# Kernel optimization log

Hardware: AMD Instinct MI355X
Metric: run time of the kernel (lower is better)

The kernel has to match this reference:

```python
import jax, jax.numpy as jnp
import numpy as np

ALPHA, BETA = 0.7, 0.3   # cost weights from match_to_memory
MARGIN = 1.0             # contrastive margin
EPS = 1e-12

N, M, D = 4096, 10240, 256

def setup_inputs() -> dict:
    key = jax.random.key(0)
    k1, k2, k3, k4, k5, k6 = jax.random.split(key, 6)
    return {
        "curr_embeds": jax.random.normal(k1, (N, D), dtype=jnp.float32),
        "curr_boxes": jax.random.uniform(k2, (N, 4), dtype=jnp.float32),
        "prev_embeds": jax.random.normal(k3, (M, D), dtype=jnp.float32),
        "prev_boxes": jax.random.uniform(k4, (M, 4), dtype=jnp.float32),
        "curr_ids": jax.random.randint(k5, (N,), 0, 5000, dtype=jnp.int64) if jax.config.read('jax_enable_x64') else jax.random.randint(k5, (N,), 0, 5000, dtype=jnp.int32),
        "prev_ids": jax.random.randint(k6, (M,), 0, 5000, dtype=jnp.int32),
    }

def _centers(boxes):
    # boxes: [K,4] as (x, y, w, h) -> centers [K,2]
    x, y, w, h = boxes[:, 0], boxes[:, 1], boxes[:, 2], boxes[:, 3]
    return jnp.stack([x + w / 2, y + h / 2], axis=-1)

def _pairwise_dist(a, b):
    # Euclidean cdist via expansion; avoids [N,M,D] intermediate.
    a2 = jnp.sum(a * a, axis=-1, keepdims=True)        # [N,1]
    b2 = jnp.sum(b * b, axis=-1, keepdims=True).T      # [1,M]
    d2 = jnp.maximum(a2 + b2 - 2.0 * (a @ b.T), 0.0)   # [N,M]
    return jnp.sqrt(d2), d2

def reference(curr_embeds, curr_boxes, prev_embeds, prev_boxes, curr_ids, prev_ids):
    # --- cost matrix (match_to_memory, pre-Hungarian) ---
    cn = curr_embeds / jnp.maximum(jnp.linalg.norm(curr_embeds, axis=1, keepdims=True), EPS)
    pn = prev_embeds / jnp.maximum(jnp.linalg.norm(prev_embeds, axis=1, keepdims=True), EPS)
    cost_sim = 1.0 - cn @ pn.T                                   # [N,M]
    cost_center, _ = _pairwise_dist(_centers(curr_boxes), _centers(prev_boxes))
    total_cost = ALPHA * cost_sim + BETA * cost_center           # [N,M]

    # --- contrastive loss (vectorized form of the O(N*M) python loop) ---
    dist, d2 = _pairwise_dist(curr_embeds, prev_embeds)          # [N,M]
    same = curr_ids[:, None] == prev_ids[None, :]                # [N,M] bool
    per_pair = jnp.where(same, d2, jnp.maximum(MARGIN - dist, 0.0) ** 2)
    loss = jnp.sum(per_pair) / (dist.shape[0] * dist.shape[1])
    return total_cost, loss
```

## Files before the change

### kernel.cpp

```cpp
#include <hip/hip_runtime.h>
#include <hip/hip_bf16.h>

#define N_CURR 4096
#define M_PREV 10240
#define DIM 256
#define BM 128
#define BN 128
#define BK2 64
#define NBX (M_PREV / BN)
#define NBY (N_CURR / BM)
#define NBLK (NBX * NBY)

typedef short short8 __attribute__((ext_vector_type(8)));
typedef float f32x4 __attribute__((ext_vector_type(4)));

__device__ __forceinline__ unsigned short f2bf(float f) {
  union { float f; unsigned int u; } x; x.f = f;
  unsigned int u = x.u;
  return (unsigned short)((u + 0x7fffu + ((u >> 16) & 1u)) >> 16);
}

__device__ __forceinline__ void async16(const void* g, void* l) {
  __builtin_amdgcn_global_load_lds(
      (const __attribute__((address_space(1))) unsigned int*)g,
      (__attribute__((address_space(3))) unsigned int*)l, 16, 0, 0);
}

__global__ __launch_bounds__(256) void prep_kernel(
    const float* __restrict__ ce, const float* __restrict__ cbx,
    const float* __restrict__ pe, const float* __restrict__ pbx,
    ushort* __restrict__ cbf, ushort* __restrict__ pbf,
    float4* __restrict__ cpar, float4* __restrict__ ppar)
{
  int gw = (blockIdx.x * 256 + threadIdx.x) >> 6;
  int lane = threadIdx.x & 63;
  bool isCurr = gw < N_CURR;
  int row = isCurr ? gw : gw - N_CURR;
  const float* src = (isCurr ? ce : pe) + (size_t)row * DIM;
  ushort* dst = (isCurr ? cbf : pbf) + (size_t)row * DIM;

  float4 v = ((const float4*)src)[lane];
  ushort4 b;
  b.x = f2bf(v.x); b.y = f2bf(v.y); b.z = f2bf(v.z); b.w = f2bf(v.w);
  ((ushort4*)dst)[lane] = b;

  float s = v.x*v.x + v.y*v.y + v.z*v.z + v.w*v.w;
  #pragma unroll
  for (int m = 32; m; m >>= 1) s += __shfl_xor(s, m);

  if (lane == 0) {
    float nrm = fmaxf(__builtin_amdgcn_sqrtf(s), 1e-12f);
    float4 bb = ((const float4*)(isCurr ? cbx : pbx))[row];
    float4 par;
    par.x = 1.0f / nrm;
    par.y = s;
    par.z = bb.x + 0.5f * bb.z;
    par.w = bb.y + 0.5f * bb.w;
    (isCurr ? cpar : ppar)[row] = par;
  }
}

__global__ __launch_bounds__(512, 4) void main_kernel(
    const ushort* __restrict__ cbf, const ushort* __restrict__ pbf,
    const float4* __restrict__ cpar, const float4* __restrict__ ppar,
    const int* __restrict__ cid, const int* __restrict__ pid,
    float* __restrict__ out, float* __restrict__ partials)
{
  __shared__ __align__(16) ushort Al[2][BM][BK2];
  __shared__ __align__(16) ushort Bl[2][BN][BK2];
  __shared__ float4 rowv[BM];
  __shared__ float4 colv[BN];
  __shared__ int ridl[BM];
  __shared__ int cidl[BN];
  __shared__ float wsum[8];

  const int bid = blockIdx.x;
  const int bx = bid % NBX;
  const int by = bid / NBX;
  const int r0 = by * BM;
  const int c0 = bx * BN;
  const int tid = threadIdx.x;
  const int lane = tid & 63;
  const int wid = tid >> 6;

  const int sr = lane >> 3;
  const int sc = ((lane & 7) ^ sr) * 8;

  auto stage = [&](int buf, int ks) {
    const int k0 = ks * BK2;
    const int rA = wid * 16 + sr;
    const ushort* gA = cbf + (size_t)(r0 + rA) * DIM + k0 + sc;
    async16(gA,           &Al[buf][wid*16][0]);
    async16(gA + 8*DIM,   &Al[buf][wid*16 + 8][0]);
    const ushort* gB = pbf + (size_t)(c0 + rA) * DIM + k0 + sc;
    async16(gB,           &Bl[buf][wid*16][0]);
    async16(gB + 8*DIM,   &Bl[buf][wid*16 + 8][0]);
  };

  stage(0, 0);

  if (tid < BM) {
    rowv[tid] = cpar[r0 + tid];
    ridl[tid] = cid[r0 + tid];
  } else if (tid < 2 * BM) {
    int t = tid - BM;
    float4 pv = ppar[c0 + t];
    pv.x *= 0.7f;
    colv[t] = pv;
    cidl[t] = pid[c0 + t];
  }

  f32x4 acc[2][4];
  #pragma unroll
  for (int n = 0; n < 2; ++n)
    #pragma unroll
    for (int m = 0; m < 4; ++m)
      acc[n][m] = (f32x4){0.f, 0.f, 0.f, 0.f};

  const int wr = wid >> 2, wc = wid & 3;
  const int rb = wr * 64, cbase = wc * 32;
  const int frow = lane & 15;
  const int f7 = frow & 7;
  const int cko = lane >> 4;

  #pragma unroll
  for (int ks = 0; ks < DIM / BK2; ++ks) {
    __syncthreads();
    if (ks < DIM / BK2 - 1) stage((ks + 1) & 1, ks + 1);
    const int buf = ks & 1;
    #pragma unroll
    for (int half = 0; half < 2; ++half) {
      const int cc = ((half * 4 + cko) ^ f7) * 16;
      short8 af[4], bfr[2];
      #pragma unroll
      for (int m = 0; m < 4; ++m)
        af[m] = *(const short8*)((const char*)&Al[buf][rb + m*16 + frow][0] + cc);
      #pragma unroll
      for (int n = 0; n < 2; ++n)
        bfr[n] = *(const short8*)((const char*)&Bl[buf][cbase + n*16 + frow][0] + cc);
      #pragma unroll
      for (int n = 0; n < 2; ++n)
        #pragma unroll
        for (int m = 0; m < 4; ++m)
          acc[n][m] = __builtin_amdgcn_mfma_f32_16x16x32_bf16(bfr[n], af[m], acc[n][m], 0, 0, 0);
    }
  }

  float lp = 0.f;
  const int g4 = (lane >> 4) << 2;
  #pragma unroll
  for (int m = 0; m < 4; ++m) {
    int il = rb + m*16 + frow;
    float4 rv = rowv[il];
    int rid = ridl[il];
    float* orow = out + (size_t)(r0 + il) * M_PREV + c0;
    #pragma unroll
    for (int n = 0; n < 2; ++n) {
      int jl0 = cbase + n*16 + g4;
      f32x4 res;
      #pragma unroll
      for (int r = 0; r < 4; ++r) {
        int jl = jl0 + r;
        float4 cv = colv[jl];
        float dot = acc[n][m][r];
        float w = rv.x * cv.x;
        float dx = rv.z - cv.z;
        float dy = rv.w - cv.w;
        float ccd = __builtin_amdgcn_sqrtf(dx*dx + dy*dy);
        res[r] = fmaf(0.3f, ccd, fmaf(-w, dot, 0.7f));
        float d2 = fmaxf(rv.y + cv.y - 2.0f * dot, 0.0f);
        float dist = __builtin_amdgcn_sqrtf(d2);
        float tt = fmaxf(1.0f - dist, 0.0f);
        lp += (rid == cidl[jl]) ? d2 : tt * tt;
      }
      *(f32x4*)(orow + jl0) = res;
    }
  }

  #pragma unroll
  for (int m = 32; m; m >>= 1) lp += __shfl_xor(lp, m);
  if (lane == 0) wsum[wid] = lp;
  __syncthreads();
  if (tid == 0) {
    float s = 0.f;
    #pragma unroll
    for (int w = 0; w < 8; ++w) s += wsum[w];
    partials[bid] = s;
  }
}

__global__ __launch_bounds__(256) void finalize_loss(
    const float* __restrict__ partials, float* __restrict__ loss_out)
{
  __shared__ float sh[4];
  float s = 0.f;
  for (int i = threadIdx.x; i < NBLK; i += 256) s += partials[i];
  #pragma unroll
  for (int m = 32; m; m >>= 1) s += __shfl_xor(s, m);
  if ((threadIdx.x & 63) == 0) sh[threadIdx.x >> 6] = s;
  __syncthreads();
  if (threadIdx.x == 0)
    loss_out[0] = ((sh[0] + sh[1]) + (sh[2] + sh[3])) * (1.0f / 41943040.0f);
}

extern "C" void kernel_launch(void* const* d_in, const int* in_sizes, int n_in,
                              void* d_out, int out_size, void* d_ws, size_t ws_size,
                              hipStream_t stream) {
  const float* ce  = (const float*)d_in[0];
  const float* cbx = (const float*)d_in[1];
  const float* pe  = (const float*)d_in[2];
  const float* pbx = (const float*)d_in[3];
  const int*   cid = (const int*)d_in[4];
  const int*   pid = (const int*)d_in[5];
  float* out = (float*)d_out;

  char* ws = (char*)d_ws;
  ushort* cbf = (ushort*)ws;
  ushort* pbf = (ushort*)(ws + (2u << 20));
  float4* cpar = (float4*)(ws + 7340032);
  float4* ppar = (float4*)(ws + 7340032 + 65536);
  float* partials = (float*)(ws + 7340032 + 65536 + 163840);

  prep_kernel<<<(N_CURR + M_PREV) / 4, 256, 0, stream>>>(
      ce, cbx, pe, pbx, cbf, pbf, cpar, ppar);
  main_kernel<<<NBLK, 512, 0, stream>>>(
      cbf, pbf, cpar, ppar, cid, pid, out, partials);
  finalize_loss<<<1, 256, 0, stream>>>(partials, out + (size_t)N_CURR * M_PREV);
}
```

Baseline: 68.55 us.

## Load B fragments directly into registers and swizzle block order across XCDs

The B operand tile no longer goes through LDS. Each wave loads its own B fragments straight from global memory into registers, double-buffered one k-step ahead. The A tile is still staged asynchronously into LDS, now synchronised with a manual vmcnt wait and a raw barrier. Block IDs are remapped so that contiguous tiles land on the same XCD, which should improve L2 reuse. The changes aim to cut LDS traffic and barrier cost, but they duplicate B global loads across the row waves, use a less coalesced access pattern, and add register pressure.

Result: slower. 83.23 us (+21.4%).

```diff
diff --git a/kernel.cpp b/kernel.cpp
--- a/kernel.cpp
+++ b/kernel.cpp
@@ -7,6 +7,7 @@
 #define BM 128
 #define BN 128
 #define BK2 64
+#define NSTEP2 (DIM / BK2)
 #define NBX (M_PREV / BN)
 #define NBY (N_CURR / BM)
 #define NBLK (NBX * NBY)
@@ -67,14 +68,13 @@
     float* __restrict__ out, float* __restrict__ partials)
 {
   __shared__ __align__(16) ushort Al[2][BM][BK2];
-  __shared__ __align__(16) ushort Bl[2][BN][BK2];
   __shared__ float4 rowv[BM];
   __shared__ float4 colv[BN];
   __shared__ int ridl[BM];
   __shared__ int cidl[BN];
   __shared__ float wsum[8];
 
-  const int bid = blockIdx.x;
+  const int bid = (blockIdx.x & 7) * (NBLK / 8) + (blockIdx.x >> 3);
   const int bx = bid % NBX;
   const int by = bid / NBX;
   const int r0 = by * BM;
@@ -83,21 +83,32 @@
   const int lane = tid & 63;
   const int wid = tid >> 6;
 
+  const int wr = wid >> 2, wc = wid & 3;
+  const int rb = wr * 64, cbase = wc * 32;
+  const int frow = lane & 15;
+  const int f7 = frow & 7;
+  const int cko = lane >> 4;
+  const int fko = (lane >> 4) * 8;
+
   const int sr = lane >> 3;
   const int sc = ((lane & 7) ^ sr) * 8;
 
-  auto stage = [&](int buf, int ks) {
+  auto stageA = [&](int buf, int ks) {
     const int k0 = ks * BK2;
-    const int rA = wid * 16 + sr;
-    const ushort* gA = cbf + (size_t)(r0 + rA) * DIM + k0 + sc;
-    async16(gA,           &Al[buf][wid*16][0]);
-    async16(gA + 8*DIM,   &Al[buf][wid*16 + 8][0]);
-    const ushort* gB = pbf + (size_t)(c0 + rA) * DIM + k0 + sc;
-    async16(gB,           &Bl[buf][wid*16][0]);
-    async16(gB + 8*DIM,   &Bl[buf][wid*16 + 8][0]);
+    const ushort* gA = cbf + (size_t)(r0 + wid*16 + sr) * DIM + k0 + sc;
+    async16(gA,         &Al[buf][wid*16][0]);
+    async16(gA + 8*DIM, &Al[buf][wid*16 + 8][0]);
   };
 
-  stage(0, 0);
+  const ushort* bBase = pbf + (size_t)(c0 + cbase + frow) * DIM + fko;
+  short8 bcur[2][2], bnxt[2][2];
+  auto loadB = [&](short8 (*dst)[2], int ks) {
+    #pragma unroll
+    for (int n = 0; n < 2; ++n)
+      #pragma unroll
+      for (int h = 0; h < 2; ++h)
+        dst[n][h] = *(const short8*)(bBase + (size_t)(n*16) * DIM + ks*BK2 + h*32);
+  };
 
   if (tid < BM) {
     rowv[tid] = cpar[r0 + tid];
@@ -109,6 +120,8 @@
     colv[t] = pv;
     cidl[t] = pid[c0 + t];
   }
+  stageA(0, 0);
+  loadB(bcur, 0);
 
   f32x4 acc[2][4];
   #pragma unroll
@@ -117,33 +130,32 @@
     for (int m = 0; m < 4; ++m)
       acc[n][m] = (f32x4){0.f, 0.f, 0.f, 0.f};
 
-  const int wr = wid >> 2, wc = wid & 3;
-  const int rb = wr * 64, cbase = wc * 32;
-  const int frow = lane & 15;
-  const int f7 = frow & 7;
-  const int cko = lane >> 4;
-
-  #pragma unroll
-  for (int ks = 0; ks < DIM / BK2; ++ks) {
-    __syncthreads();
-    if (ks < DIM / BK2 - 1) stage((ks + 1) & 1, ks + 1);
+  #pragma unroll
+  for (int ks = 0; ks < NSTEP2; ++ks) {
+    asm volatile("s_waitcnt vmcnt(4)" ::: "memory");
+    __builtin_amdgcn_s_barrier();
+    __builtin_amdgcn_sched_barrier(0);
+    if (ks + 1 < NSTEP2) stageA((ks + 1) & 1, ks + 1);
+    if (ks + 1 < NSTEP2) loadB(bnxt, ks + 1);
     const int buf = ks & 1;
     #pragma unroll
-    for (int half = 0; half < 2; ++half) {
-      const int cc = ((half * 4 + cko) ^ f7) * 16;
-      short8 af[4], bfr[2];
+    for (int h = 0; h < 2; ++h) {
+      const int cc = ((h * 4 + cko) ^ f7) * 16;
+      short8 af[4];
       #pragma unroll
       for (int m = 0; m < 4; ++m)
         af[m] = *(const short8*)((const char*)&Al[buf][rb + m*16 + frow][0] + cc);
-      #pragma unroll
-      for (int n = 0; n < 2; ++n)
-        bfr[n] = *(const short8*)((const char*)&Bl[buf][cbase + n*16 + frow][0] + cc);
       #pragma unroll
       for (int n = 0; n < 2; ++n)
         #pragma unroll
         for (int m = 0; m < 4; ++m)
-          acc[n][m] = __builtin_amdgcn_mfma_f32_16x16x32_bf16(bfr[n], af[m], acc[n][m], 0, 0, 0);
+          acc[n][m] = __builtin_amdgcn_mfma_f32_16x16x32_bf16(bcur[n][h], af[m], acc[n][m], 0, 0, 0);
     }
+    #pragma unroll
+    for (int n = 0; n < 2; ++n)
+      #pragma unroll
+      for (int h = 0; h < 2; ++h)
+        bcur[n][h] = bnxt[n][h];
   }
 
   float lp = 0.f;
@@ -168,7 +180,7 @@
         float dy = rv.w - cv.w;
         float ccd = __builtin_amdgcn_sqrtf(dx*dx + dy*dy);
         res[r] = fmaf(0.3f, ccd, fmaf(-w, dot, 0.7f));
-        float d2 = fmaxf(rv.y + cv.y - 2.0f * dot, 0.0f);
+        float d2 = fmaxf(fmaf(-2.0f, dot, rv.y + cv.y), 0.0f);
         float dist = __builtin_amdgcn_sqrtf(d2);
         float tt = fmaxf(1.0f - dist, 0.0f);
         lp += (rid == cidl[jl]) ? d2 : tt * tt;
```
